# Kernel tuning notes

Measured on AMD Instinct MI355X. Metric: run time of the kernel, lower is better.

The kernel has to match this reference:

```python
import jax, jax.numpy as jnp
import numpy as np

C = 256        # conv_dim / hidden_size
VOC = 106      # voc_size + 1
MAX_LEN = 25   # num_chars
GROUPS = 32


def setup_inputs() -> dict:
    key = jax.random.key(0)
    ks = jax.random.split(key, 32)
    s = 0.05
    d = {}
    d['rois'] = jax.random.normal(ks[0], (64, C, 16, 128), jnp.float32)
    d['conv1_w'] = jax.random.normal(ks[1], (C, C, 3, 3), jnp.float32) * s
    d['gn1_g'] = jnp.ones((C,), jnp.float32)
    d['gn1_b'] = jnp.zeros((C,), jnp.float32)
    d['conv2_w'] = jax.random.normal(ks[2], (C, C, 3, 3), jnp.float32) * s
    d['gn2_g'] = jnp.ones((C,), jnp.float32)
    d['gn2_b'] = jnp.zeros((C,), jnp.float32)
    # BiLSTM (nIn=C, nHidden=C), PyTorch gate order i,f,g,o
    d['lstm_wih_f'] = jax.random.normal(ks[3], (4 * C, C), jnp.float32) * s
    d['lstm_whh_f'] = jax.random.normal(ks[4], (4 * C, C), jnp.float32) * s
    d['lstm_bih_f'] = jnp.zeros((4 * C,), jnp.float32)
    d['lstm_bhh_f'] = jnp.zeros((4 * C,), jnp.float32)
    d['lstm_wih_b'] = jax.random.normal(ks[5], (4 * C, C), jnp.float32) * s
    d['lstm_whh_b'] = jax.random.normal(ks[6], (4 * C, C), jnp.float32) * s
    d['lstm_bih_b'] = jnp.zeros((4 * C,), jnp.float32)
    d['lstm_bhh_b'] = jnp.zeros((4 * C,), jnp.float32)
    d['emb_w'] = jax.random.normal(ks[7], (C, 2 * C), jnp.float32) * s   # 2H -> C projection
    d['emb_b'] = jnp.zeros((C,), jnp.float32)
    # Attention decoder params
    d['att_emb'] = jax.random.normal(ks[8], (VOC, C), jnp.float32) * s   # char embedding table
    d['comb_w'] = jax.random.normal(ks[9], (C, 2 * C), jnp.float32) * s  # attn_combine
    d['comb_b'] = jnp.zeros((C,), jnp.float32)
    d['gru_wih'] = jax.random.normal(ks[10], (3 * C, C), jnp.float32) * s  # gates r,z,n
    d['gru_whh'] = jax.random.normal(ks[11], (3 * C, C), jnp.float32) * s
    d['gru_bih'] = jnp.zeros((3 * C,), jnp.float32)
    d['gru_bhh'] = jnp.zeros((3 * C,), jnp.float32)
    d['out_w'] = jax.random.normal(ks[12], (VOC, C), jnp.float32) * s
    d['out_b'] = jnp.zeros((VOC,), jnp.float32)
    d['vat_w'] = jax.random.normal(ks[13], (1, C), jnp.float32) * s
    d['vat_b'] = jnp.zeros((1,), jnp.float32)
    return d


def _group_norm(x, g, b, eps=1e-5):
    N, Ch, H, W = x.shape
    xg = x.reshape(N, GROUPS, Ch // GROUPS, H, W)
    m = xg.mean(axis=(2, 3, 4), keepdims=True)
    v = xg.var(axis=(2, 3, 4), keepdims=True)
    xn = ((xg - m) / jnp.sqrt(v + eps)).reshape(N, Ch, H, W)
    return xn * g[None, :, None, None] + b[None, :, None, None]


def _conv_gn_relu(x, w, g, b):
    y = jax.lax.conv_general_dilated(x, w, window_strides=(2, 1),
                                     padding=((1, 1), (1, 1)),
                                     dimension_numbers=('NCHW', 'OIHW', 'NCHW'))
    return jax.nn.relu(_group_norm(y, g, b))


def _lstm_dir(x, Wih, Whh, bih, bhh, reverse):
    # x: (T, N, C) -> hidden states (T, N, H)
    N = x.shape[1]
    Hd = Whh.shape[1]
    def step(carry, xt):
        h, c = carry
        gates = xt @ Wih.T + h @ Whh.T + (bih + bhh)
        i, f, gg, o = jnp.split(gates, 4, axis=-1)
        c = jax.nn.sigmoid(f) * c + jax.nn.sigmoid(i) * jnp.tanh(gg)
        h = jax.nn.sigmoid(o) * jnp.tanh(c)
        return (h, c), h
    init = (jnp.zeros((N, Hd), x.dtype), jnp.zeros((N, Hd), x.dtype))
    _, hs = jax.lax.scan(step, init, x, reverse=reverse)
    return hs


def _forward(rois, conv1_w, gn1_g, gn1_b, conv2_w, gn2_g, gn2_b,
             lstm_wih_f, lstm_whh_f, lstm_bih_f, lstm_bhh_f,
             lstm_wih_b, lstm_whh_b, lstm_bih_b, lstm_bhh_b,
             emb_w, emb_b, att_emb, comb_w, comb_b,
             gru_wih, gru_whh, gru_bih, gru_bhh, out_w, out_b, vat_w, vat_b):
    # CRNN encoder
    x = _conv_gn_relu(rois, conv1_w, gn1_g, gn1_b)
    x = _conv_gn_relu(x, conv2_w, gn2_g, gn2_b)
    x = x.mean(axis=2)                      # (N, C, W)
    x = jnp.transpose(x, (2, 0, 1))         # (T, N, C)
    fw = _lstm_dir(x, lstm_wih_f, lstm_whh_f, lstm_bih_f, lstm_bhh_f, False)
    bw = _lstm_dir(x, lstm_wih_b, lstm_whh_b, lstm_bih_b, lstm_bhh_b, True)
    rec = jnp.concatenate([fw, bw], axis=-1)        # (T, N, 2C)
    enc = rec @ emb_w.T + emb_b                     # (T, N, C) encoder_outputs

    n = enc.shape[1]

    def dec_step(carry, _):
        inp, h = carry                              # inp: (n,) int, h: (n, C)
        e = att_emb[inp]                            # embedding (dropout = identity at eval)
        alpha = jnp.tanh(h[None, :, :] + enc)       # (T, n, C)
        aw = jnp.squeeze(alpha @ vat_w.T, -1) + vat_b[0]  # (T, n)
        aw = jax.nn.softmax(aw, axis=0)             # softmax over time
        ctx = jnp.einsum('tn,tnc->nc', aw, enc)     # attn_applied
        o = jax.nn.relu(jnp.concatenate([e, ctx], axis=-1) @ comb_w.T + comb_b)
        gi = o @ gru_wih.T + gru_bih
        gh = h @ gru_whh.T + gru_bhh
        ir, iz, innw = jnp.split(gi, 3, axis=-1)
        hr, hz, hn = jnp.split(gh, 3, axis=-1)
        r = jax.nn.sigmoid(ir + hr)
        z = jax.nn.sigmoid(iz + hz)
        nn_ = jnp.tanh(innw + r * hn)
        h2 = (1.0 - z) * nn_ + z * h
        logits = jax.nn.log_softmax(h2 @ out_w.T + out_b, axis=-1)
        ni = jnp.argmax(logits, axis=-1)            # greedy feedback
        return (ni, h2), logits

    init = (jnp.zeros((n,), jnp.int32), jnp.zeros((n, C), enc.dtype))
    _, outs = jax.lax.scan(dec_step, init, None, length=MAX_LEN)
    return jnp.transpose(outs, (1, 0, 2))           # decoder_raw: (n, MAX_LEN, VOC)


def reference(rois, conv1_w, gn1_g, gn1_b, conv2_w, gn2_g, gn2_b,
              lstm_wih_f, lstm_whh_f, lstm_bih_f, lstm_bhh_f,
              lstm_wih_b, lstm_whh_b, lstm_bih_b, lstm_bhh_b,
              emb_w, emb_b, att_emb, comb_w, comb_b,
              gru_wih, gru_whh, gru_bih, gru_bhh, out_w, out_b, vat_w, vat_b):
    return _forward(rois, conv1_w, gn1_g, gn1_b, conv2_w, gn2_g, gn2_b,
                    lstm_wih_f, lstm_whh_f, lstm_bih_f, lstm_bhh_f,
                    lstm_wih_b, lstm_whh_b, lstm_bih_b, lstm_bhh_b,
                    emb_w, emb_b, att_emb, comb_w, comb_b,
                    gru_wih, gru_whh, gru_bih, gru_bhh, out_w, out_b, vat_w, vat_b)
```

## Files before the change

kernel.cpp:

```cpp
#include <hip/hip_runtime.h>
#include <cstdint>

typedef unsigned short u16;
typedef unsigned int   u32;
typedef __attribute__((ext_vector_type(8))) __bf16 bf16x8;
typedef __attribute__((ext_vector_type(4))) float  f32x4;

#define DEV static __device__ __forceinline__

DEV float bf2f(u16 u) { union { u32 i; float f; } v; v.i = ((u32)u) << 16; return v.f; }
DEV u16 f2bf(float f) {
  union { float f; u32 i; } v; v.f = f;
  u32 x = v.i;
  x += 0x7fffu + ((x >> 16) & 1u);
  return (u16)(x >> 16);
}
DEV void splitf(float x, u16 &h, u16 &l) { h = f2bf(x); float r = x - bf2f(h); l = f2bf(r); }
DEV float sigm(float x) { return 1.f / (1.f + __expf(-x)); }
DEV float tanh_(float x) { float e = __expf(2.f * x); return 1.f - 2.f / (e + 1.f); }
DEV f32x4 mfma_bf16(bf16x8 a, bf16x8 b, f32x4 c) {
  return __builtin_amdgcn_mfma_f32_16x16x32_bf16(a, b, c, 0, 0, 0);
}

__global__ __launch_bounds__(256) void k_repack_convw(const float* __restrict__ w,
                                                      u16* __restrict__ oh, u16* __restrict__ ol) {
  int idx = blockIdx.x * 256 + threadIdx.x;
  if (idx >= 256 * 2304) return;
  int co = idx / 2304, r = idx - co * 2304;
  int seg = r >> 8, ci = r & 255;
  float v = w[(co * 256 + ci) * 9 + seg];
  u16 h, l; splitf(v, h, l);
  oh[idx] = h; ol[idx] = l;
}

__global__ __launch_bounds__(256) void k_split(const float* __restrict__ s,
                                               u16* __restrict__ h, u16* __restrict__ l, int count) {
  int i = blockIdx.x * 256 + threadIdx.x;
  if (i < count) { u16 a, b; splitf(s[i], a, b); h[i] = a; l[i] = b; }
}

template <int H_OUT, int H_IN, int MODE>
__global__ __launch_bounds__(256)
void k_conv_gemm(const float* __restrict__ Ain, const u16* __restrict__ Bth, const u16* __restrict__ Btl,
                 float* __restrict__ Out, const float* __restrict__ gstat,
                 const float* __restrict__ gamma, const float* __restrict__ beta) {
  __shared__ __align__(16) u16 Ash[128 * 32];
  __shared__ __align__(16) u16 Asl[128 * 32];
  __shared__ __align__(16) u16 Bsh[128 * 32];
  __shared__ __align__(16) u16 Bsl[128 * 32];
  const int tid = threadIdx.x;
  const int bx = blockIdx.x, ct = blockIdx.y;
  const int n = bx / H_OUT, hp = bx % H_OUT;
  const int wid = tid >> 6, lane = tid & 63;
  const int wr = wid >> 1, wc = wid & 1;
  const int lr = lane & 15, lk = lane >> 4;
  const int iw = tid & 127, chalf = tid >> 7;
  f32x4 acc[4][4] = {};
  for (int step = 0; step < 72; ++step) {
    const int seg = step >> 3, ci0 = (step & 7) << 5;
    const int kh = seg / 3, kw = seg - kh * 3;
    const int ih = 2 * hp + kh - 1;
    const int iws = iw + kw - 1;
    const bool ok = (ih >= 0) && (ih < H_IN) && (iws >= 0) && (iws < 128);
#pragma unroll
    for (int j = 0; j < 2; ++j) {
      int chunk = j * 256 + tid;
      int row = chunk >> 2, sub = chunk & 3;
      int off = (ct * 128 + row) * 2304 + step * 32 + sub * 8;
      *(uint4*)&Bsh[chunk * 8] = *(const uint4*)&Bth[off];
      *(uint4*)&Bsl[chunk * 8] = *(const uint4*)&Btl[off];
    }
    if constexpr (MODE == 0) {
      const float* src = Ain + (((long)(n * 256 + ci0) * H_IN + ih) * 128 + iws);
#pragma unroll
      for (int g8 = 0; g8 < 2; ++g8) {
        u32 ph[4], pl[4];
#pragma unroll
        for (int q = 0; q < 4; ++q) {
          int c = chalf * 16 + g8 * 8 + q * 2;
          float v0 = 0.f, v1 = 0.f;
          if (ok) { v0 = src[(long)c * (H_IN * 128)]; v1 = src[(long)(c + 1) * (H_IN * 128)]; }
          u16 h0, l0, h1, l1; splitf(v0, h0, l0); splitf(v1, h1, l1);
          ph[q] = (u32)h0 | ((u32)h1 << 16);
          pl[q] = (u32)l0 | ((u32)l1 << 16);
        }
        *(uint4*)&Ash[iw * 32 + chalf * 16 + g8 * 8] = make_uint4(ph[0], ph[1], ph[2], ph[3]);
        *(uint4*)&Asl[iw * 32 + chalf * 16 + g8 * 8] = make_uint4(pl[0], pl[1], pl[2], pl[3]);
      }
    } else {
      const float* src = Ain + ((((long)n * H_IN + ih) * 128 + iws) * 256 + ci0 + chalf * 16);
#pragma unroll
      for (int g8 = 0; g8 < 2; ++g8) {
        int c0 = ci0 + chalf * 16 + g8 * 8;
        int g = c0 >> 3;
        float m = gstat[(n * 32 + g) * 2], rs = gstat[(n * 32 + g) * 2 + 1];
        float x[8] = {};
        if (ok) {
          float4 a = *(const float4*)(src + g8 * 8);
          float4 b = *(const float4*)(src + g8 * 8 + 4);
          x[0] = a.x; x[1] = a.y; x[2] = a.z; x[3] = a.w;
          x[4] = b.x; x[5] = b.y; x[6] = b.z; x[7] = b.w;
        }
        u32 ph[4], pl[4];
#pragma unroll
        for (int q = 0; q < 4; ++q) {
          int c = c0 + q * 2;
          float v0 = ok ? fmaxf((x[q * 2]     - m) * rs * gamma[c]     + beta[c],     0.f) : 0.f;
          float v1 = ok ? fmaxf((x[q * 2 + 1] - m) * rs * gamma[c + 1] + beta[c + 1], 0.f) : 0.f;
          u16 h0, l0, h1, l1; splitf(v0, h0, l0); splitf(v1, h1, l1);
          ph[q] = (u32)h0 | ((u32)h1 << 16);
          pl[q] = (u32)l0 | ((u32)l1 << 16);
        }
        *(uint4*)&Ash[iw * 32 + chalf * 16 + g8 * 8] = make_uint4(ph[0], ph[1], ph[2], ph[3]);
        *(uint4*)&Asl[iw * 32 + chalf * 16 + g8 * 8] = make_uint4(pl[0], pl[1], pl[2], pl[3]);
      }
    }
    __syncthreads();
    bf16x8 ah[4], al[4], bh[4], bl[4];
#pragma unroll
    for (int mi = 0; mi < 4; ++mi) {
      int row = wr * 64 + mi * 16 + lr;
      ah[mi] = *(const bf16x8*)&Ash[row * 32 + lk * 8];
      al[mi] = *(const bf16x8*)&Asl[row * 32 + lk * 8];
    }
#pragma unroll
    for (int ni = 0; ni < 4; ++ni) {
      int row = wc * 64 + ni * 16 + lr;
      bh[ni] = *(const bf16x8*)&Bsh[row * 32 + lk * 8];
      bl[ni] = *(const bf16x8*)&Bsl[row * 32 + lk * 8];
    }
#pragma unroll
    for (int mi = 0; mi < 4; ++mi)
#pragma unroll
      for (int ni = 0; ni < 4; ++ni) {
        f32x4 c = acc[mi][ni];
        c = mfma_bf16(al[mi], bh[ni], c);
        c = mfma_bf16(ah[mi], bl[ni], c);
        c = mfma_bf16(ah[mi], bh[ni], c);
        acc[mi][ni] = c;
      }
    __syncthreads();
  }
#pragma unroll
  for (int mi = 0; mi < 4; ++mi)
#pragma unroll
    for (int ni = 0; ni < 4; ++ni)
#pragma unroll
      for (int r = 0; r < 4; ++r) {
        int w = wr * 64 + mi * 16 + lk * 4 + r;
        int co = ct * 128 + wc * 64 + ni * 16 + lr;
        Out[(((long)(n * H_OUT + hp)) * 128 + w) * 256 + co] = acc[mi][ni][r];
      }
}

__global__ __launch_bounds__(256)
void k_gemm_split(const u16* __restrict__ Ah, const u16* __restrict__ Al,
                  const u16* __restrict__ Bh, const u16* __restrict__ Bl,
                  float* __restrict__ outF, const float* __restrict__ bias, int K) {
  __shared__ __align__(16) u16 Ash[128 * 32];
  __shared__ __align__(16) u16 Asl[128 * 32];
  __shared__ __align__(16) u16 Bsh[128 * 32];
  __shared__ __align__(16) u16 Bsl[128 * 32];
  const int tid = threadIdx.x;
  const int m0 = blockIdx.x * 128, n0 = blockIdx.y * 128;
  const int N = gridDim.y * 128;
  const int wid = tid >> 6, lane = tid & 63;
  const int wr = wid >> 1, wc = wid & 1;
  const int lr = lane & 15, lk = lane >> 4;
  f32x4 acc[4][4] = {};
  const int steps = K >> 5;
  for (int s = 0; s < steps; ++s) {
    const int k0 = s << 5;
#pragma unroll
    for (int j = 0; j < 2; ++j) {
      int chunk = j * 256 + tid;
      int row = chunk >> 2, sub = chunk & 3;
      long aoff = (long)(m0 + row) * K + k0 + sub * 8;
      long boff = (long)(n0 + row) * K + k0 + sub * 8;
      *(uint4*)&Ash[chunk * 8] = *(const uint4*)&Ah[aoff];
      *(uint4*)&Asl[chunk * 8] = *(const uint4*)&Al[aoff];
      *(uint4*)&Bsh[chunk * 8] = *(const uint4*)&Bh[boff];
      *(uint4*)&Bsl[chunk * 8] = *(const uint4*)&Bl[boff];
    }
    __syncthreads();
    bf16x8 ah[4], al[4], bh[4], bl[4];
#pragma unroll
    for (int mi = 0; mi < 4; ++mi) {
      int row = wr * 64 + mi * 16 + lr;
      ah[mi] = *(const bf16x8*)&Ash[row * 32 + lk * 8];
      al[mi] = *(const bf16x8*)&Asl[row * 32 + lk * 8];
    }
#pragma unroll
    for (int ni = 0; ni < 4; ++ni) {
      int row = wc * 64 + ni * 16 + lr;
      bh[ni] = *(const bf16x8*)&Bsh[row * 32 + lk * 8];
      bl[ni] = *(const bf16x8*)&Bsl[row * 32 + lk * 8];
    }
#pragma unroll
    for (int mi = 0; mi < 4; ++mi)
#pragma unroll
      for (int ni = 0; ni < 4; ++ni) {
        f32x4 c = acc[mi][ni];
        c = mfma_bf16(al[mi], bh[ni], c);
        c = mfma_bf16(ah[mi], bl[ni], c);
        c = mfma_bf16(ah[mi], bh[ni], c);
        acc[mi][ni] = c;
      }
    __syncthreads();
  }
#pragma unroll
  for (int mi = 0; mi < 4; ++mi)
#pragma unroll
    for (int ni = 0; ni < 4; ++ni)
#pragma unroll
      for (int r = 0; r < 4; ++r) {
        int m = m0 + wr * 64 + mi * 16 + lk * 4 + r;
        int col = n0 + wc * 64 + ni * 16 + lr;
        float v = acc[mi][ni][r];
        if (bias) v += bias[col];
        outF[(long)m * N + col] = v;
      }
}

__global__ __launch_bounds__(256)
void k_gemm_gx(const u16* __restrict__ Ah, const u16* __restrict__ Al,
               const u16* __restrict__ Bh, const u16* __restrict__ Bl,
               float* __restrict__ outF) {
  __shared__ __align__(16) u16 Ash[128 * 32];
  __shared__ __align__(16) u16 Asl[128 * 32];
  __shared__ __align__(16) u16 Bsh[128 * 32];
  __shared__ __align__(16) u16 Bsl[128 * 32];
  const int tid = threadIdx.x;
  const int m0 = blockIdx.x * 128, n0 = blockIdx.y * 128;
  const int K = 256;
  const int wid = tid >> 6, lane = tid & 63;
  const int wr = wid >> 1, wc = wid & 1;
  const int lr = lane & 15, lk = lane >> 4;
  f32x4 acc[4][4] = {};
  for (int s = 0; s < 8; ++s) {
    const int k0 = s << 5;
#pragma unroll
    for (int j = 0; j < 2; ++j) {
      int chunk = j * 256 + tid;
      int row = chunk >> 2, sub = chunk & 3;
      long aoff = (long)(m0 + row) * K + k0 + sub * 8;
      long boff = (long)(n0 + row) * K + k0 + sub * 8;
      *(uint4*)&Ash[chunk * 8] = *(const uint4*)&Ah[aoff];
      *(uint4*)&Asl[chunk * 8] = *(const uint4*)&Al[aoff];
      *(uint4*)&Bsh[chunk * 8] = *(const uint4*)&Bh[boff];
      *(uint4*)&Bsl[chunk * 8] = *(const uint4*)&Bl[boff];
    }
    __syncthreads();
    bf16x8 ah[4], al[4], bh[4], bl[4];
#pragma unroll
    for (int mi = 0; mi < 4; ++mi) {
      int row = wr * 64 + mi * 16 + lr;
      ah[mi] = *(const bf16x8*)&Ash[row * 32 + lk * 8];
      al[mi] = *(const bf16x8*)&Asl[row * 32 + lk * 8];
    }
#pragma unroll
    for (int ni = 0; ni < 4; ++ni) {
      int row = wc * 64 + ni * 16 + lr;
      bh[ni] = *(const bf16x8*)&Bsh[row * 32 + lk * 8];
      bl[ni] = *(const bf16x8*)&Bsl[row * 32 + lk * 8];
    }
#pragma unroll
    for (int mi = 0; mi < 4; ++mi)
#pragma unroll
      for (int ni = 0; ni < 4; ++ni) {
        f32x4 c = acc[mi][ni];
        c = mfma_bf16(al[mi], bh[ni], c);
        c = mfma_bf16(ah[mi], bl[ni], c);
        c = mfma_bf16(ah[mi], bh[ni], c);
        acc[mi][ni] = c;
      }
    __syncthreads();
  }
#pragma unroll
  for (int mi = 0; mi < 4; ++mi)
#pragma unroll
    for (int ni = 0; ni < 4; ++ni) {
      int t = blockIdx.x * 2 + wr;
      int nbase = mi * 16 + lk * 4;
      int col = n0 + wc * 64 + ni * 16 + lr;
      int gate = col >> 8, u = col & 255;
      int prow = ((u >> 4) << 6) + (gate << 4) + (u & 15);
      float4 st = make_float4(acc[mi][ni][0], acc[mi][ni][1], acc[mi][ni][2], acc[mi][ni][3]);
      *(float4*)&outF[((long)t * 1024 + prow) * 64 + nbase] = st;
    }
}

__global__ __launch_bounds__(256)
void k_gn_stats(const float* __restrict__ y, float* __restrict__ stat, int H) {
  const int n = blockIdx.x >> 5, g = blockIdx.x & 31;
  const int tid = threadIdx.x;
  const int cnt = H * 128;
  float s = 0.f, q = 0.f;
  for (int i = tid; i < cnt; i += 256) {
    int h = i >> 7, w = i & 127;
    const float4* p = (const float4*)(y + (((long)(n * H + h) * 128 + w) * 256 + g * 8));
    float4 a = p[0], b = p[1];
    s += a.x + a.y + a.z + a.w + b.x + b.y + b.z + b.w;
    q += a.x * a.x + a.y * a.y + a.z * a.z + a.w * a.w + b.x * b.x + b.y * b.y + b.z * b.z + b.w * b.w;
  }
  __shared__ float rs_[256], rq_[256];
  rs_[tid] = s; rq_[tid] = q; __syncthreads();
  for (int off = 128; off > 0; off >>= 1) {
    if (tid < off) { rs_[tid] += rs_[tid + off]; rq_[tid] += rq_[tid + off]; }
    __syncthreads();
  }
  if (tid == 0) {
    float c = (float)(cnt * 8);
    float m = rs_[0] / c;
    float var = rq_[0] / c - m * m;
    stat[(n * 32 + g) * 2] = m;
    stat[(n * 32 + g) * 2 + 1] = rsqrtf(var + 1e-5f);
  }
}

__global__ __launch_bounds__(256)
void k_xbuild(const float* __restrict__ out2, const float* __restrict__ stat,
              const float* __restrict__ gamma, const float* __restrict__ beta,
              u16* __restrict__ xh, u16* __restrict__ xl) {
  int idx = blockIdx.x * 256 + threadIdx.x;
  int c = idx & 255;
  int n = (idx >> 8) & 63;
  int t = idx >> 14;
  int g = c >> 3;
  float m = stat[(n * 32 + g) * 2], rs = stat[(n * 32 + g) * 2 + 1];
  float ga = gamma[c], be = beta[c];
  float acc = 0.f;
#pragma unroll
  for (int h = 0; h < 4; ++h) {
    float v = out2[(((long)(n * 4 + h) * 128 + t) * 256) + c];
    acc += fmaxf((v - m) * rs * ga + be, 0.f);
  }
  acc *= 0.25f;
  u16 a, b; splitf(acc, a, b);
  xh[idx] = a; xl[idx] = b;
}

__global__ __launch_bounds__(256)
void k_lstm_mfma(const float* __restrict__ gxPf, const float* __restrict__ gxPb,
                 const float* __restrict__ whhf, const float* __restrict__ whhb,
                 const float* __restrict__ bihf, const float* __restrict__ bhhf,
                 const float* __restrict__ bihb, const float* __restrict__ bhhb,
                 u16* __restrict__ hHi, u16* __restrict__ hLo,
                 u16* __restrict__ hsH, u16* __restrict__ hsL,
                 int* __restrict__ bar) {
  __shared__ __align__(16) u16 WH[64 * 256];
  __shared__ __align__(16) u16 WL[64 * 256];
  const int tid = threadIdx.x;
  const int dir = blockIdx.x >> 4;
  const int b   = blockIdx.x & 15;
  const float* whh = dir ? whhb : whhf;
  const float* bih = dir ? bihb : bihf;
  const float* bhh = dir ? bhhb : bhhf;
  const float* gxP = dir ? gxPb : gxPf;
  for (int i = tid; i < 4096; i += 256) {
    int r = i >> 6;
    int kc = (i & 63) << 2;
    int gate = r >> 4, uu = r & 15;
    const float* src = whh + ((long)(gate * 256 + b * 16 + uu)) * 256 + kc;
    float4 v = *(const float4*)src;
    u16 h0, l0, h1, l1, h2, l2, h3, l3;
    splitf(v.x, h0, l0); splitf(v.y, h1, l1); splitf(v.z, h2, l2); splitf(v.w, h3, l3);
    int byte = (r << 9) + (kc << 1);
    byte ^= (r & 7) << 4;
    *(ushort4*)((char*)WH + byte) = make_ushort4(h0, h1, h2, h3);
    *(ushort4*)((char*)WL + byte) = make_ushort4(l0, l1, l2, l3);
  }
  const int wid = tid >> 6, lane = tid & 63;
  const int lr = lane & 15, lk = lane >> 4;
  const int n0 = wid * 16;
  const int u = b * 16 + lr;
  float bias4[4];
#pragma unroll
  for (int g = 0; g < 4; ++g) {
    int row = g * 256 + u;
    bias4[g] = bih[row] + bhh[row];
  }
  float creg[4] = {0.f, 0.f, 0.f, 0.f};
  const char* WHc = (const char*)WH;
  const char* WLc = (const char*)WL;
  __syncthreads();
  for (int s = 0; s < 128; ++s) {
    const int t = dir ? (127 - s) : s;
    const int rb = s & 1, wb = rb ^ 1;
    const u16* hrH = hHi + (size_t)((rb * 2 + dir) * 64) * 256;
    const u16* hrL = hLo + (size_t)((rb * 2 + dir) * 64) * 256;
    f32x4 acc[4] = {};
#pragma unroll
    for (int ks = 0; ks < 8; ++ks) {
      bf16x8 ah = *(const bf16x8*)&hrH[(n0 + lr) * 256 + ks * 32 + lk * 8];
      bf16x8 al = *(const bf16x8*)&hrL[(n0 + lr) * 256 + ks * 32 + lk * 8];
#pragma unroll
      for (int ni = 0; ni < 4; ++ni) {
        int byte = ((ni * 16 + lr) << 9) + (ks << 6) + (lk << 4);
        byte ^= (lr & 7) << 4;
        bf16x8 bh = *(const bf16x8*)(WHc + byte);
        bf16x8 bl = *(const bf16x8*)(WLc + byte);
        f32x4 c = acc[ni];
        c = mfma_bf16(al, bh, c);
        c = mfma_bf16(ah, bl, c);
        c = mfma_bf16(ah, bh, c);
        acc[ni] = c;
      }
    }
    float4 gx[4];
#pragma unroll
    for (int ni = 0; ni < 4; ++ni)
      gx[ni] = *(const float4*)&gxP[((long)t * 1024 + b * 64 + ni * 16 + lr) * 64 + n0 + lk * 4];
    u16* hwH = hHi + (size_t)((wb * 2 + dir) * 64) * 256;
    u16* hwL = hLo + (size_t)((wb * 2 + dir) * 64) * 256;
#pragma unroll
    for (int r = 0; r < 4; ++r) {
      float iv = sigm(acc[0][r] + ((const float*)&gx[0])[r] + bias4[0]);
      float fv = sigm(acc[1][r] + ((const float*)&gx[1])[r] + bias4[1]);
      float gv = tanh_(acc[2][r] + ((const float*)&gx[2])[r] + bias4[2]);
      float ov = sigm(acc[3][r] + ((const float*)&gx[3])[r] + bias4[3]);
      creg[r] = fv * creg[r] + iv * gv;
      float hv = ov * tanh_(creg[r]);
      u16 hh, hl; splitf(hv, hh, hl);
      int n = n0 + lk * 4 + r;
      hwH[n * 256 + u] = hh;
      hwL[n * 256 + u] = hl;
      size_t o = ((size_t)(t * 64 + n)) * 512 + dir * 256 + u;
      hsH[o] = hh; hsL[o] = hl;
    }
    __syncthreads();
    if (tid == 0) {
      __hip_atomic_fetch_add(&bar[dir], 1, __ATOMIC_ACQ_REL, __HIP_MEMORY_SCOPE_AGENT);
      const int target = (s + 1) * 16;
      while (__hip_atomic_load(&bar[dir], __ATOMIC_RELAXED, __HIP_MEMORY_SCOPE_AGENT) < target)
        __builtin_amdgcn_s_sleep(1);
    }
    __syncthreads();
    __threadfence();
  }
}

__global__ __launch_bounds__(256)
void k_decoder(const float* __restrict__ enc, const float* __restrict__ att_emb,
               const float* __restrict__ comb_w, const float* __restrict__ comb_b,
               const float* __restrict__ gru_wih, const float* __restrict__ gru_whh,
               const float* __restrict__ gru_bih, const float* __restrict__ gru_bhh,
               const float* __restrict__ out_w, const float* __restrict__ out_b,
               const float* __restrict__ vat_w, float* __restrict__ dout) {
  const int n = blockIdx.x, tid = threadIdx.x;
  __shared__ float hsh[256], esh[256], ctx[256], osh[256], vsh[256];
  __shared__ float sc[128], lg[128];
  __shared__ float red[256];
  __shared__ int redi[256];
  __shared__ int inp_sh;
  hsh[tid] = 0.f;
  vsh[tid] = vat_w[tid];
  if (tid == 0) inp_sh = 0;
  __syncthreads();
  for (int step = 0; step < 25; ++step) {
    esh[tid] = att_emb[inp_sh * 256 + tid];
    {
      const int t = tid >> 1, hf = tid & 1;
      const float* ep = enc + ((t * 64 + n) * 256 + hf * 128);
      const float* hp = hsh + hf * 128;
      const float* vp = vsh + hf * 128;
      float a = 0.f;
      for (int k = 0; k < 128; ++k) a += tanh_(hp[k] + ep[k]) * vp[k];
      a += __shfl_xor(a, 1);
      if (hf == 0) sc[t] = a;
    }
    __syncthreads();
    red[tid] = (tid < 128) ? sc[tid] : -3.0e38f;
    __syncthreads();
    for (int off = 128; off >= 1; off >>= 1) {
      if (tid < off) red[tid] = fmaxf(red[tid], red[tid + off]);
      __syncthreads();
    }
    const float smax = red[0];
    __syncthreads();
    {
      float e = (tid < 128) ? __expf(sc[tid] - smax) : 0.f;
      if (tid < 128) sc[tid] = e;
      red[tid] = e;
    }
    __syncthreads();
    for (int off = 128; off >= 1; off >>= 1) {
      if (tid < off) red[tid] += red[tid + off];
      __syncthreads();
    }
    const float sinv = 1.f / red[0];
    __syncthreads();
    {
      float a = 0.f;
      for (int t = 0; t < 128; ++t) a += sc[t] * enc[(t * 64 + n) * 256 + tid];
      ctx[tid] = a * sinv;
    }
    __syncthreads();
    {
      const float* w = comb_w + (long)tid * 512;
      float a = comb_b[tid];
      for (int k = 0; k < 256; k += 4) {
        float4 wv = *(const float4*)(w + k);
        a += esh[k] * wv.x + esh[k + 1] * wv.y + esh[k + 2] * wv.z + esh[k + 3] * wv.w;
      }
      for (int k = 0; k < 256; k += 4) {
        float4 wv = *(const float4*)(w + 256 + k);
        a += ctx[k] * wv.x + ctx[k + 1] * wv.y + ctx[k + 2] * wv.z + ctx[k + 3] * wv.w;
      }
      osh[tid] = fmaxf(a, 0.f);
    }
    __syncthreads();
    float h2;
    {
      const float* wir = gru_wih + (long)tid * 256;
      const float* wiz = gru_wih + (long)(256 + tid) * 256;
      const float* win = gru_wih + (long)(512 + tid) * 256;
      const float* whr = gru_whh + (long)tid * 256;
      const float* whz = gru_whh + (long)(256 + tid) * 256;
      const float* whn = gru_whh + (long)(512 + tid) * 256;
      float ar = gru_bih[tid], az = gru_bih[256 + tid], an = gru_bih[512 + tid];
      float br = gru_bhh[tid], bz = gru_bhh[256 + tid], bn = gru_bhh[512 + tid];
      for (int k = 0; k < 256; k += 4) {
        float4 o4 = *(const float4*)&osh[k];
        float4 h4 = *(const float4*)&hsh[k];
        float4 w;
        w = *(const float4*)(wir + k); ar += o4.x * w.x + o4.y * w.y + o4.z * w.z + o4.w * w.w;
        w = *(const float4*)(wiz + k); az += o4.x * w.x + o4.y * w.y + o4.z * w.z + o4.w * w.w;
        w = *(const float4*)(win + k); an += o4.x * w.x + o4.y * w.y + o4.z * w.z + o4.w * w.w;
        w = *(const float4*)(whr + k); br += h4.x * w.x + h4.y * w.y + h4.z * w.z + h4.w * w.w;
        w = *(const float4*)(whz + k); bz += h4.x * w.x + h4.y * w.y + h4.z * w.z + h4.w * w.w;
        w = *(const float4*)(whn + k); bn += h4.x * w.x + h4.y * w.y + h4.z * w.z + h4.w * w.w;
      }
      float r = sigm(ar + br);
      float z = sigm(az + bz);
      float nn = tanh_(an + r * bn);
      h2 = (1.f - z) * nn + z * hsh[tid];
    }
    __syncthreads();
    hsh[tid] = h2;
    __syncthreads();
    {
      float l = -3.0e38f;
      if (tid < 106) {
        const float* w = out_w + (long)tid * 256;
        float a = out_b[tid];
        for (int k = 0; k < 256; k += 4) {
          float4 h4 = *(const float4*)&hsh[k];
          float4 wv = *(const float4*)(w + k);
          a += h4.x * wv.x + h4.y * wv.y + h4.z * wv.z + h4.w * wv.w;
        }
        l = a; lg[tid] = a;
      }
      red[tid] = l;
      redi[tid] = (tid < 106) ? tid : 0x7FFFFFFF;
      __syncthreads();
      for (int off = 128; off >= 1; off >>= 1) {
        if (tid < off) {
          float v2 = red[tid + off]; int i2 = redi[tid + off];
          if (v2 > red[tid] || (v2 == red[tid] && i2 < redi[tid])) { red[tid] = v2; redi[tid] = i2; }
        }
        __syncthreads();
      }
      const float lmax = red[0];
      const int amax = redi[0];
      __syncthreads();
      red[tid] = (tid < 106) ? __expf(lg[tid] - lmax) : 0.f;
      __syncthreads();
      for (int off = 128; off >= 1; off >>= 1) {
        if (tid < off) red[tid] += red[tid + off];
        __syncthreads();
      }
      const float lse = lmax + __logf(red[0]);
      if (tid < 106) dout[((long)n * 25 + step) * 106 + tid] = lg[tid] - lse;
      if (tid == 0) inp_sh = amax;
    }
    __syncthreads();
  }
}

extern "C" void kernel_launch(void* const* d_in, const int* in_sizes, int n_in,
                              void* d_out, int out_size, void* d_ws, size_t ws_size,
                              hipStream_t stream) {
  (void)in_sizes; (void)n_in; (void)out_size;
  const float* rois    = (const float*)d_in[0];
  const float* conv1_w = (const float*)d_in[1];
  const float* gn1_g   = (const float*)d_in[2];
  const float* gn1_b   = (const float*)d_in[3];
  const float* conv2_w = (const float*)d_in[4];
  const float* gn2_g   = (const float*)d_in[5];
  const float* gn2_b   = (const float*)d_in[6];
  const float* wih_f   = (const float*)d_in[7];
  const float* whh_f   = (const float*)d_in[8];
  const float* bih_f   = (const float*)d_in[9];
  const float* bhh_f   = (const float*)d_in[10];
  const float* wih_b   = (const float*)d_in[11];
  const float* whh_b   = (const float*)d_in[12];
  const float* bih_b   = (const float*)d_in[13];
  const float* bhh_b   = (const float*)d_in[14];
  const float* emb_w   = (const float*)d_in[15];
  const float* emb_b   = (const float*)d_in[16];
  const float* att_emb = (const float*)d_in[17];
  const float* comb_w  = (const float*)d_in[18];
  const float* comb_b  = (const float*)d_in[19];
  const float* gru_wih = (const float*)d_in[20];
  const float* gru_whh = (const float*)d_in[21];
  const float* gru_bih = (const float*)d_in[22];
  const float* gru_bhh = (const float*)d_in[23];
  const float* out_w   = (const float*)d_in[24];
  const float* out_b   = (const float*)d_in[25];
  const float* vat_w   = (const float*)d_in[26];

  if (ws_size < 116686864u) return;
  char* ws = (char*)d_ws;
  float* OUT1  = (float*)(ws + 0);
  float* GXF   = (float*)(ws + 0);
  float* GXB   = (float*)(ws + 33554432);
  float* OUT2  = (float*)(ws + 67108864);
  u16*   HSH_  = (u16*)  (ws + 67108864);
  u16*   HSL_  = (u16*)  (ws + 75497472);
  float* ENC   = (float*)(ws + 83886080);
  u16*   XBH   = (u16*)  (ws + 100663296);
  u16*   XBL   = (u16*)  (ws + 104857600);
  u16*   W1TH  = (u16*)  (ws + 109051904);
  u16*   W1TL  = (u16*)  (ws + 110231552);
  u16*   W2TH  = (u16*)  (ws + 111411200);
  u16*   W2TL  = (u16*)  (ws + 112590848);
  u16*   WIHFH = (u16*)  (ws + 113770496);
  u16*   WIHFL = (u16*)  (ws + 114294784);
  u16*   WIHBH = (u16*)  (ws + 114819072);
  u16*   WIHBL = (u16*)  (ws + 115343360);
  u16*   EMBWH = (u16*)  (ws + 115867648);
  u16*   EMBWL = (u16*)  (ws + 116129792);
  float* GN1S  = (float*)(ws + 116391936);
  float* GN2S  = (float*)(ws + 116408320);
  u16*   HBUFH = (u16*)  (ws + 116424704);
  u16*   HBUFL = (u16*)  (ws + 116555776);
  int*   BAR   = (int*)  (ws + 116686848);

  hipMemsetAsync(HBUFH, 0, 131072, stream);
  hipMemsetAsync(HBUFL, 0, 131072, stream);
  hipMemsetAsync(BAR, 0, 16, stream);

  k_repack_convw<<<2304, 256, 0, stream>>>(conv1_w, W1TH, W1TL);
  k_repack_convw<<<2304, 256, 0, stream>>>(conv2_w, W2TH, W2TL);
  k_split<<<1024, 256, 0, stream>>>(wih_f, WIHFH, WIHFL, 262144);
  k_split<<<1024, 256, 0, stream>>>(wih_b, WIHBH, WIHBL, 262144);
  k_split<<<512, 256, 0, stream>>>(emb_w, EMBWH, EMBWL, 131072);

  k_conv_gemm<8, 16, 0><<<dim3(512, 2), 256, 0, stream>>>(rois, W1TH, W1TL, OUT1, nullptr, nullptr, nullptr);
  k_gn_stats<<<2048, 256, 0, stream>>>(OUT1, GN1S, 8);
  k_conv_gemm<4, 8, 1><<<dim3(256, 2), 256, 0, stream>>>(OUT1, W2TH, W2TL, OUT2, GN1S, gn1_g, gn1_b);
  k_gn_stats<<<2048, 256, 0, stream>>>(OUT2, GN2S, 4);
  k_xbuild<<<8192, 256, 0, stream>>>(OUT2, GN2S, gn2_g, gn2_b, XBH, XBL);

  k_gemm_gx<<<dim3(64, 8), 256, 0, stream>>>(XBH, XBL, WIHFH, WIHFL, GXF);
  k_gemm_gx<<<dim3(64, 8), 256, 0, stream>>>(XBH, XBL, WIHBH, WIHBL, GXB);
  k_lstm_mfma<<<32, 256, 0, stream>>>(GXF, GXB, whh_f, whh_b, bih_f, bhh_f, bih_b, bhh_b,
                                      HBUFH, HBUFL, HSH_, HSL_, BAR);
  k_gemm_split<<<dim3(64, 2), 256, 0, stream>>>(HSH_, HSL_, EMBWH, EMBWL, ENC, emb_b, 512);

  k_decoder<<<64, 256, 0, stream>>>(ENC, att_emb, comb_w, comb_b, gru_wih, gru_whh,
                                    gru_bih, gru_bhh, out_w, out_b, vat_w, (float*)d_out);
}
```

Measured before the change: 4.003 ms.

## Halve LSTM blocks with wider per-block units and widen decoder to 1024 threads

The recurrent LSTM kernel now runs 8 blocks per direction instead of 16. Each block owns 32 hidden units, doubling its weight tile in LDS to 128 KB. This halves the number of participants in the per-step grid barrier, and the next timestep's input-gate values are prefetched into registers while the current step computes. The decoder kernel now uses 1024 threads per block, splitting the attention, combine, GRU and output dot products across more threads. Its shared-memory tree reductions are replaced by wave shuffle reductions to cut serial sync chains per decode step. The cost is less parallelism per LSTM step and more per-block MFMA work and LDS use, so occupancy may be limited.

Result: slower. 4.218 ms (+5.4%).

```diff
diff --git a/kernel.cpp b/kernel.cpp
--- a/kernel.cpp
+++ b/kernel.cpp
@@ -348,20 +348,20 @@
                  u16* __restrict__ hHi, u16* __restrict__ hLo,
                  u16* __restrict__ hsH, u16* __restrict__ hsL,
                  int* __restrict__ bar) {
-  __shared__ __align__(16) u16 WH[64 * 256];
-  __shared__ __align__(16) u16 WL[64 * 256];
+  __shared__ __align__(16) u16 WH[128 * 256];
+  __shared__ __align__(16) u16 WL[128 * 256];
   const int tid = threadIdx.x;
-  const int dir = blockIdx.x >> 4;
-  const int b   = blockIdx.x & 15;
+  const int dir = blockIdx.x >> 3;
+  const int b   = blockIdx.x & 7;
   const float* whh = dir ? whhb : whhf;
   const float* bih = dir ? bihb : bihf;
   const float* bhh = dir ? bhhb : bhhf;
   const float* gxP = dir ? gxPb : gxPf;
-  for (int i = tid; i < 4096; i += 256) {
+  for (int i = tid; i < 8192; i += 256) {
     int r = i >> 6;
     int kc = (i & 63) << 2;
-    int gate = r >> 4, uu = r & 15;
-    const float* src = whh + ((long)(gate * 256 + b * 16 + uu)) * 256 + kc;
+    int gate = r >> 5, uu = r & 31;
+    const float* src = whh + ((long)(gate * 256 + b * 32 + uu)) * 256 + kc;
     float4 v = *(const float4*)src;
     u16 h0, l0, h1, l1, h2, l2, h3, l3;
     splitf(v.x, h0, l0); splitf(v.y, h1, l1); splitf(v.z, h2, l2); splitf(v.w, h3, l3);
@@ -373,29 +373,39 @@
   const int wid = tid >> 6, lane = tid & 63;
   const int lr = lane & 15, lk = lane >> 4;
   const int n0 = wid * 16;
-  const int u = b * 16 + lr;
-  float bias4[4];
-#pragma unroll
-  for (int g = 0; g < 4; ++g) {
-    int row = g * 256 + u;
-    bias4[g] = bih[row] + bhh[row];
-  }
-  float creg[4] = {0.f, 0.f, 0.f, 0.f};
+  float bias_[2][4];
+#pragma unroll
+  for (int uh = 0; uh < 2; ++uh)
+#pragma unroll
+    for (int g = 0; g < 4; ++g) {
+      int row = g * 256 + b * 32 + uh * 16 + lr;
+      bias_[uh][g] = bih[row] + bhh[row];
+    }
+  float creg[2][4] = {};
   const char* WHc = (const char*)WH;
   const char* WLc = (const char*)WL;
+  float4 gxc[2][4];
+  {
+    const int t0 = dir ? 127 : 0;
+#pragma unroll
+    for (int uh = 0; uh < 2; ++uh)
+#pragma unroll
+      for (int g = 0; g < 4; ++g)
+        gxc[uh][g] = *(const float4*)&gxP[((size_t)t0 * 1024 + (b * 2 + uh) * 64 + g * 16 + lr) * 64 + n0 + lk * 4];
+  }
   __syncthreads();
   for (int s = 0; s < 128; ++s) {
     const int t = dir ? (127 - s) : s;
     const int rb = s & 1, wb = rb ^ 1;
     const u16* hrH = hHi + (size_t)((rb * 2 + dir) * 64) * 256;
     const u16* hrL = hLo + (size_t)((rb * 2 + dir) * 64) * 256;
-    f32x4 acc[4] = {};
+    f32x4 acc[8] = {};
 #pragma unroll
     for (int ks = 0; ks < 8; ++ks) {
       bf16x8 ah = *(const bf16x8*)&hrH[(n0 + lr) * 256 + ks * 32 + lk * 8];
       bf16x8 al = *(const bf16x8*)&hrL[(n0 + lr) * 256 + ks * 32 + lk * 8];
 #pragma unroll
-      for (int ni = 0; ni < 4; ++ni) {
+      for (int ni = 0; ni < 8; ++ni) {
         int byte = ((ni * 16 + lr) << 9) + (ks << 6) + (lk << 4);
         byte ^= (lr & 7) << 4;
         bf16x8 bh = *(const bf16x8*)(WHc + byte);
@@ -407,31 +417,47 @@
         acc[ni] = c;
       }
     }
-    float4 gx[4];
-#pragma unroll
-    for (int ni = 0; ni < 4; ++ni)
-      gx[ni] = *(const float4*)&gxP[((long)t * 1024 + b * 64 + ni * 16 + lr) * 64 + n0 + lk * 4];
+    float4 gxn[2][4];
+    if (s < 127) {
+      const int tn = dir ? (126 - s) : (s + 1);
+#pragma unroll
+      for (int uh = 0; uh < 2; ++uh)
+#pragma unroll
+        for (int g = 0; g < 4; ++g)
+          gxn[uh][g] = *(const float4*)&gxP[((size_t)tn * 1024 + (b * 2 + uh) * 64 + g * 16 + lr) * 64 + n0 + lk * 4];
+    }
     u16* hwH = hHi + (size_t)((wb * 2 + dir) * 64) * 256;
     u16* hwL = hLo + (size_t)((wb * 2 + dir) * 64) * 256;
 #pragma unroll
-    for (int r = 0; r < 4; ++r) {
-      float iv = sigm(acc[0][r] + ((const float*)&gx[0])[r] + bias4[0]);
-      float fv = sigm(acc[1][r] + ((const float*)&gx[1])[r] + bias4[1]);
-      float gv = tanh_(acc[2][r] + ((const float*)&gx[2])[r] + bias4[2]);
-      float ov = sigm(acc[3][r] + ((const float*)&gx[3])[r] + bias4[3]);
-      creg[r] = fv * creg[r] + iv * gv;
-      float hv = ov * tanh_(creg[r]);
-      u16 hh, hl; splitf(hv, hh, hl);
-      int n = n0 + lk * 4 + r;
-      hwH[n * 256 + u] = hh;
-      hwL[n * 256 + u] = hl;
-      size_t o = ((size_t)(t * 64 + n)) * 512 + dir * 256 + u;
-      hsH[o] = hh; hsL[o] = hl;
+    for (int uh = 0; uh < 2; ++uh) {
+      const int u = b * 32 + uh * 16 + lr;
+#pragma unroll
+      for (int r = 0; r < 4; ++r) {
+        float iv = sigm(acc[0 * 2 + uh][r] + ((const float*)&gxc[uh][0])[r] + bias_[uh][0]);
+        float fv = sigm(acc[1 * 2 + uh][r] + ((const float*)&gxc[uh][1])[r] + bias_[uh][1]);
+        float gv = tanh_(acc[2 * 2 + uh][r] + ((const float*)&gxc[uh][2])[r] + bias_[uh][2]);
+        float ov = sigm(acc[3 * 2 + uh][r] + ((const float*)&gxc[uh][3])[r] + bias_[uh][3]);
+        creg[uh][r] = fv * creg[uh][r] + iv * gv;
+        float hv = ov * tanh_(creg[uh][r]);
+        u16 hh, hl; splitf(hv, hh, hl);
+        int n = n0 + lk * 4 + r;
+        hwH[n * 256 + u] = hh;
+        hwL[n * 256 + u] = hl;
+        size_t o = ((size_t)(t * 64 + n)) * 512 + dir * 256 + u;
+        hsH[o] = hh; hsL[o] = hl;
+      }
+    }
+    if (s < 127) {
+#pragma unroll
+      for (int uh = 0; uh < 2; ++uh)
+#pragma unroll
+        for (int g = 0; g < 4; ++g)
+          gxc[uh][g] = gxn[uh][g];
     }
     __syncthreads();
     if (tid == 0) {
       __hip_atomic_fetch_add(&bar[dir], 1, __ATOMIC_ACQ_REL, __HIP_MEMORY_SCOPE_AGENT);
-      const int target = (s + 1) * 16;
+      const int target = (s + 1) * 8;
       while (__hip_atomic_load(&bar[dir], __ATOMIC_RELAXED, __HIP_MEMORY_SCOPE_AGENT) < target)
         __builtin_amdgcn_s_sleep(1);
     }
@@ -440,7 +466,7 @@
   }
 }
 
-__global__ __launch_bounds__(256)
+__global__ __launch_bounds__(1024)
 void k_decoder(const float* __restrict__ enc, const float* __restrict__ att_emb,
                const float* __restrict__ comb_w, const float* __restrict__ comb_b,
                const float* __restrict__ gru_wih, const float* __restrict__ gru_whh,
@@ -450,130 +476,135 @@
   const int n = blockIdx.x, tid = threadIdx.x;
   __shared__ float hsh[256], esh[256], ctx[256], osh[256], vsh[256];
   __shared__ float sc[128], lg[128];
-  __shared__ float red[256];
-  __shared__ int redi[256];
+  __shared__ float part[1024];
+  __shared__ float gp[1536];
+  __shared__ float op[1024];
+  __shared__ float sca[2];
   __shared__ int inp_sh;
-  hsh[tid] = 0.f;
-  vsh[tid] = vat_w[tid];
+  if (tid < 256) { hsh[tid] = 0.f; vsh[tid] = vat_w[tid]; }
   if (tid == 0) inp_sh = 0;
   __syncthreads();
   for (int step = 0; step < 25; ++step) {
-    esh[tid] = att_emb[inp_sh * 256 + tid];
+    if (tid < 256) esh[tid] = att_emb[inp_sh * 256 + tid];
     {
-      const int t = tid >> 1, hf = tid & 1;
-      const float* ep = enc + ((t * 64 + n) * 256 + hf * 128);
-      const float* hp = hsh + hf * 128;
-      const float* vp = vsh + hf * 128;
+      const int t = tid >> 3, kq = tid & 7;
+      const float* ep = enc + ((t * 64 + n) * 256 + kq * 32);
+      const float* hp = hsh + kq * 32;
+      const float* vp = vsh + kq * 32;
       float a = 0.f;
-      for (int k = 0; k < 128; ++k) a += tanh_(hp[k] + ep[k]) * vp[k];
-      a += __shfl_xor(a, 1);
-      if (hf == 0) sc[t] = a;
-    }
-    __syncthreads();
-    red[tid] = (tid < 128) ? sc[tid] : -3.0e38f;
-    __syncthreads();
-    for (int off = 128; off >= 1; off >>= 1) {
-      if (tid < off) red[tid] = fmaxf(red[tid], red[tid + off]);
-      __syncthreads();
-    }
-    const float smax = red[0];
-    __syncthreads();
+#pragma unroll
+      for (int k0 = 0; k0 < 32; ++k0) {
+        int k = (k0 + kq * 4) & 31;
+        a += tanh_(hp[k] + ep[k]) * vp[k];
+      }
+      a += __shfl_xor(a, 1); a += __shfl_xor(a, 2); a += __shfl_xor(a, 4);
+      if (kq == 0) sc[t] = a;
+    }
+    __syncthreads();
+    if (tid < 64) {
+      float v0 = sc[tid], v1 = sc[tid + 64];
+      float m = fmaxf(v0, v1);
+      for (int w = 1; w < 64; w <<= 1) m = fmaxf(m, __shfl_xor(m, w));
+      float e0 = __expf(v0 - m), e1 = __expf(v1 - m);
+      sc[tid] = e0; sc[tid + 64] = e1;
+      float ss = e0 + e1;
+      for (int w = 1; w < 64; w <<= 1) ss += __shfl_xor(ss, w);
+      if (tid == 0) sca[0] = 1.f / ss;
+    }
+    __syncthreads();
+    const float sinv = sca[0];
     {
-      float e = (tid < 128) ? __expf(sc[tid] - smax) : 0.f;
-      if (tid < 128) sc[tid] = e;
-      red[tid] = e;
-    }
-    __syncthreads();
-    for (int off = 128; off >= 1; off >>= 1) {
-      if (tid < off) red[tid] += red[tid + off];
-      __syncthreads();
-    }
-    const float sinv = 1.f / red[0];
+      const int c = tid & 255, tq = tid >> 8;
+      const float* ep = enc + (((tq * 32) * 64 + n) * 256 + c);
+      float a = 0.f;
+#pragma unroll 4
+      for (int t2 = 0; t2 < 32; ++t2) a += sc[tq * 32 + t2] * ep[(size_t)t2 * 16384];
+      part[tq * 256 + c] = a;
+    }
+    __syncthreads();
+    if (tid < 256) ctx[tid] = (part[tid] + part[256 + tid] + part[512 + tid] + part[768 + tid]) * sinv;
     __syncthreads();
     {
+      const int u = tid & 255, kq = tid >> 8;
+      const float* w = comb_w + (size_t)u * 512 + kq * 128;
+      const float* src = (kq < 2) ? (esh + kq * 128) : (ctx + (kq - 2) * 128);
       float a = 0.f;
-      for (int t = 0; t < 128; ++t) a += sc[t] * enc[(t * 64 + n) * 256 + tid];
-      ctx[tid] = a * sinv;
-    }
+      for (int k = 0; k < 128; k += 4) {
+        float4 wv = *(const float4*)(w + k);
+        a += src[k] * wv.x + src[k + 1] * wv.y + src[k + 2] * wv.z + src[k + 3] * wv.w;
+      }
+      part[kq * 256 + u] = a;
+    }
+    __syncthreads();
+    if (tid < 256)
+      osh[tid] = fmaxf(part[tid] + part[256 + tid] + part[512 + tid] + part[768 + tid] + comb_b[tid], 0.f);
     __syncthreads();
     {
-      const float* w = comb_w + (long)tid * 512;
-      float a = comb_b[tid];
+      const int u = tid & 255, m = tid >> 8;
+      const float* w1; const float* s1;
+      if (m == 0)      { w1 = gru_wih + (size_t)u * 256;         s1 = osh; }
+      else if (m == 1) { w1 = gru_wih + (size_t)(256 + u) * 256; s1 = osh; }
+      else if (m == 2) { w1 = gru_wih + (size_t)(512 + u) * 256; s1 = osh; }
+      else             { w1 = gru_whh + (size_t)u * 256;         s1 = hsh; }
+      float a = 0.f;
       for (int k = 0; k < 256; k += 4) {
-        float4 wv = *(const float4*)(w + k);
-        a += esh[k] * wv.x + esh[k + 1] * wv.y + esh[k + 2] * wv.z + esh[k + 3] * wv.w;
-      }
-      for (int k = 0; k < 256; k += 4) {
-        float4 wv = *(const float4*)(w + 256 + k);
-        a += ctx[k] * wv.x + ctx[k + 1] * wv.y + ctx[k + 2] * wv.z + ctx[k + 3] * wv.w;
-      }
-      osh[tid] = fmaxf(a, 0.f);
-    }
-    __syncthreads();
-    float h2;
+        float4 wv = *(const float4*)(w1 + k);
+        a += s1[k] * wv.x + s1[k + 1] * wv.y + s1[k + 2] * wv.z + s1[k + 3] * wv.w;
+      }
+      gp[m * 256 + u] = a;
+      if (m < 2) {
+        const float* w2 = gru_whh + (size_t)((m + 1) * 256 + u) * 256;
+        float a2 = 0.f;
+        for (int k = 0; k < 256; k += 4) {
+          float4 wv = *(const float4*)(w2 + k);
+          a2 += hsh[k] * wv.x + hsh[k + 1] * wv.y + hsh[k + 2] * wv.z + hsh[k + 3] * wv.w;
+        }
+        gp[(4 + m) * 256 + u] = a2;
+      }
+    }
+    __syncthreads();
+    if (tid < 256) {
+      float r  = sigm(gp[tid] + gru_bih[tid] + gp[768 + tid] + gru_bhh[tid]);
+      float z  = sigm(gp[256 + tid] + gru_bih[256 + tid] + gp[1024 + tid] + gru_bhh[256 + tid]);
+      float nn = tanh_(gp[512 + tid] + gru_bih[512 + tid] + r * (gp[1280 + tid] + gru_bhh[512 + tid]));
+      hsh[tid] = (1.f - z) * nn + z * hsh[tid];
+    }
+    __syncthreads();
     {
-      const float* wir = gru_wih + (long)tid * 256;
-      const float* wiz = gru_wih + (long)(256 + tid) * 256;
-      const float* win = gru_wih + (long)(512 + tid) * 256;
-      const float* whr = gru_whh + (long)tid * 256;
-      const float* whz = gru_whh + (long)(256 + tid) * 256;
-      const float* whn = gru_whh + (long)(512 + tid) * 256;
-      float ar = gru_bih[tid], az = gru_bih[256 + tid], an = gru_bih[512 + tid];
-      float br = gru_bhh[tid], bz = gru_bhh[256 + tid], bn = gru_bhh[512 + tid];
-      for (int k = 0; k < 256; k += 4) {
-        float4 o4 = *(const float4*)&osh[k];
-        float4 h4 = *(const float4*)&hsh[k];
-        float4 w;
-        w = *(const float4*)(wir + k); ar += o4.x * w.x + o4.y * w.y + o4.z * w.z + o4.w * w.w;
-        w = *(const float4*)(wiz + k); az += o4.x * w.x + o4.y * w.y + o4.z * w.z + o4.w * w.w;
-        w = *(const float4*)(win + k); an += o4.x * w.x + o4.y * w.y + o4.z * w.z + o4.w * w.w;
-        w = *(const float4*)(whr + k); br += h4.x * w.x + h4.y * w.y + h4.z * w.z + h4.w * w.w;
-        w = *(const float4*)(whz + k); bz += h4.x * w.x + h4.y * w.y + h4.z * w.z + h4.w * w.w;
-        w = *(const float4*)(whn + k); bn += h4.x * w.x + h4.y * w.y + h4.z * w.z + h4.w * w.w;
-      }
-      float r = sigm(ar + br);
-      float z = sigm(az + bz);
-      float nn = tanh_(an + r * bn);
-      h2 = (1.f - z) * nn + z * hsh[tid];
-    }
-    __syncthreads();
-    hsh[tid] = h2;
-    __syncthreads();
-    {
-      float l = -3.0e38f;
-      if (tid < 106) {
-        const float* w = out_w + (long)tid * 256;
-        float a = out_b[tid];
-        for (int k = 0; k < 256; k += 4) {
-          float4 h4 = *(const float4*)&hsh[k];
+      const int u = tid & 127, kq = tid >> 7;
+      float a = 0.f;
+      if (u < 106) {
+        const float* w = out_w + (size_t)u * 256 + kq * 32;
+        const float* hp = hsh + kq * 32;
+        for (int k = 0; k < 32; k += 4) {
           float4 wv = *(const float4*)(w + k);
-          a += h4.x * wv.x + h4.y * wv.y + h4.z * wv.z + h4.w * wv.w;
+          a += hp[k] * wv.x + hp[k + 1] * wv.y + hp[k + 2] * wv.z + hp[k + 3] * wv.w;
         }
-        l = a; lg[tid] = a;
-      }
-      red[tid] = l;
-      redi[tid] = (tid < 106) ? tid : 0x7FFFFFFF;
-      __syncthreads();
-      for (int off = 128; off >= 1; off >>= 1) {
-        if (tid < off) {
-          float v2 = red[tid + off]; int i2 = redi[tid + off];
-          if (v2 > red[tid] || (v2 == red[tid] && i2 < redi[tid])) { red[tid] = v2; redi[tid] = i2; }
-        }
-        __syncthreads();
-      }
-      const float lmax = red[0];
-      const int amax = redi[0];
-      __syncthreads();
-      red[tid] = (tid < 106) ? __expf(lg[tid] - lmax) : 0.f;
-      __syncthreads();
-      for (int off = 128; off >= 1; off >>= 1) {
-        if (tid < off) red[tid] += red[tid + off];
-        __syncthreads();
-      }
-      const float lse = lmax + __logf(red[0]);
-      if (tid < 106) dout[((long)n * 25 + step) * 106 + tid] = lg[tid] - lse;
-      if (tid == 0) inp_sh = amax;
-    }
+      }
+      op[kq * 128 + u] = a;
+    }
+    __syncthreads();
+    if (tid < 128) {
+      float a = op[tid] + op[128 + tid] + op[256 + tid] + op[384 + tid]
+              + op[512 + tid] + op[640 + tid] + op[768 + tid] + op[896 + tid];
+      lg[tid] = (tid < 106) ? (a + out_b[tid]) : -3.0e38f;
+    }
+    __syncthreads();
+    if (tid < 64) {
+      float v0 = lg[tid];
+      float v1 = lg[tid + 64];
+      float m; int im;
+      if (v1 > v0) { m = v1; im = tid + 64; } else { m = v0; im = tid; }
+      for (int w = 1; w < 64; w <<= 1) {
+        float mo = __shfl_xor(m, w); int io = __shfl_xor(im, w);
+        if (mo > m || (mo == m && io < im)) { m = mo; im = io; }
+      }
+      float e = __expf(v0 - m) + ((tid + 64 < 106) ? __expf(v1 - m) : 0.f);
+      for (int w = 1; w < 64; w <<= 1) e += __shfl_xor(e, w);
+      if (tid == 0) { sca[0] = m + __logf(e); inp_sh = im; }
+    }
+    __syncthreads();
+    if (tid < 106) dout[((size_t)n * 25 + step) * 106 + tid] = lg[tid] - sca[0];
     __syncthreads();
   }
 }
@@ -655,10 +686,10 @@
 
   k_gemm_gx<<<dim3(64, 8), 256, 0, stream>>>(XBH, XBL, WIHFH, WIHFL, GXF);
   k_gemm_gx<<<dim3(64, 8), 256, 0, stream>>>(XBH, XBL, WIHBH, WIHBL, GXB);
-  k_lstm_mfma<<<32, 256, 0, stream>>>(GXF, GXB, whh_f, whh_b, bih_f, bhh_f, bih_b, bhh_b,
+  k_lstm_mfma<<<16, 256, 0, stream>>>(GXF, GXB, whh_f, whh_b, bih_f, bhh_f, bih_b, bhh_b,
                                       HBUFH, HBUFL, HSH_, HSL_, BAR);
   k_gemm_split<<<dim3(64, 2), 256, 0, stream>>>(HSH_, HSL_, EMBWH, EMBWL, ENC, emb_b, 512);
 
-  k_decoder<<<64, 256, 0, stream>>>(ENC, att_emb, comb_w, comb_b, gru_wih, gru_whh,
-                                    gru_bih, gru_bhh, out_w, out_b, vat_w, (float*)d_out);
-}
+  k_decoder<<<64, 1024, 0, stream>>>(ENC, att_emb, comb_w, comb_b, gru_wih, gru_whh,
+                                     gru_bih, gru_bhh, out_w, out_b, vat_w, (float*)d_out);
+}
```
